# Kernel optimization log

Hardware: AMD Instinct MI355X
Metric: run time of the kernel (lower is better)

Reference implementation:

```python
import jax, jax.numpy as jnp
import numpy as np

NUM_USER = 50000
NUM_ITEM = 50000
DIM_FEAT = 4096
DIM_LATENT = 128
NUM_LAYER = 2
AVG_DEG = 16
N = NUM_USER + NUM_ITEM
E_HALF = NUM_USER * AVG_DEG  # user->item edges; reversed copies added too


def setup_inputs() -> dict:
    key = jax.random.key(0)
    ks = jax.random.split(key, 6)
    features = jax.random.normal(ks[0], (NUM_ITEM, DIM_FEAT), dtype=jnp.float32)
    # xavier_normal for preference: std = sqrt(2/(fan_in+fan_out))
    preference = jax.random.normal(ks[1], (NUM_USER, DIM_LATENT), dtype=jnp.float32) * np.sqrt(2.0 / (NUM_USER + DIM_LATENT)).astype(np.float32)
    W1 = jax.random.normal(ks[2], (DIM_FEAT, 4 * DIM_LATENT), dtype=jnp.float32) * np.float32(DIM_FEAT ** -0.5)
    b1 = jnp.zeros((4 * DIM_LATENT,), jnp.float32)
    W2 = jax.random.normal(ks[3], (4 * DIM_LATENT, DIM_LATENT), dtype=jnp.float32) * np.float32((4 * DIM_LATENT) ** -0.5)
    b2 = jnp.zeros((DIM_LATENT,), jnp.float32)
    # bipartite user-item edges, both directions; no self-loops by construction
    u = jax.random.randint(ks[4], (E_HALF,), 0, NUM_USER)
    it = jax.random.randint(ks[5], (E_HALF,), NUM_USER, N)
    src = jnp.concatenate([u, it])
    dst = jnp.concatenate([it, u])
    edge_index = jnp.stack([src, dst], axis=0)
    return {"features": features, "preference": preference, "W1": W1, "b1": b1,
            "W2": W2, "b2": b2, "edge_index": edge_index}


def reference(features, preference, W1, b1, W2, b2, edge_index):
    # proj MLP: Linear -> LeakyReLU(0.01) -> Linear
    item_feat = jax.nn.leaky_relu(features @ W1 + b1, negative_slope=0.01) @ W2 + b2
    x = jnp.concatenate([preference, item_feat], axis=0)  # [N, D]
    # F.normalize(x, dim=-1): divide by L2 norm clamped to 1e-12
    x = x / jnp.maximum(jnp.linalg.norm(x, axis=-1, keepdims=True), 1e-12)
    row, col = edge_index[0], edge_index[1]  # source (j), target (i)
    # degree over source index only, as in BaseGCN.message
    deg = jax.ops.segment_sum(jnp.ones(row.shape[0], dtype=x.dtype), row, num_segments=N)
    deg_inv_sqrt = deg ** -0.5  # endpoints all appear as sources, so finite on edges
    norm = deg_inv_sqrt[row] * deg_inv_sqrt[col]  # [E]
    out = x
    h = x
    for _ in range(NUM_LAYER):
        msg = norm[:, None] * h[row]                      # gather + scale [E, D]
        h = jax.ops.segment_sum(msg, col, num_segments=N)  # scatter-add [N, D]
        out = out + h
    return out, preference
```

## Files before the change

### kernel.cpp

```cpp
#include <hip/hip_runtime.h>

#define NUSER 50000
#define NITEM 50000
#define NTOT  100000
#define DFEAT 4096
#define DLAT  128
#define DHID  512
#define MTILES 391
#define MPAD  (MTILES*128)
#define G1TILES 782

typedef __attribute__((ext_vector_type(8))) short bf16x8;
typedef __attribute__((ext_vector_type(4))) float f32x4;

__device__ __forceinline__ ushort f2bf(float f) {
  union { float f; unsigned u; } in; in.f = f;
  unsigned u = in.u;
  u += 0x7fffu + ((u >> 16) & 1u);
  return (ushort)(u >> 16);
}
__device__ __forceinline__ unsigned pk2bf_fast(float lo, float hi) {
  unsigned ul = __float_as_uint(lo) + 0x8000u;
  unsigned uh = __float_as_uint(hi) + 0x8000u;
  return (ul >> 16) | (uh & 0xffff0000u);
}

__global__ __launch_bounds__(512) void gemm1_kernel(
    const float* __restrict__ A,
    const ushort* __restrict__ BT,
    const float* __restrict__ bias,
    ushort* __restrict__ Hid)
{
  extern __shared__ char smem[];
  char* AsC = smem;
  char* BsC = smem + 8192;

  const int tid = threadIdx.x;
  const int lane = tid & 63;
  const int wid = tid >> 6;
  const int row0 = blockIdx.x * 64;

  const int lr = lane & 15;
  const int kq = lane >> 4;
  const int l7 = lane & 7;

  f32x4 acc[4][4];
  const f32x4 z = {0.f, 0.f, 0.f, 0.f};
  #pragma unroll
  for (int m = 0; m < 4; ++m)
    #pragma unroll
    for (int n = 0; n < 4; ++n) acc[m][n] = z;

  const int r0 = tid >> 3, t0 = tid & 7;
  const int aswz = (t0 ^ (r0 & 7)) << 4;
  const size_t asrc = (size_t)(row0 + r0) * DFEAT + t0 * 8;
  char* adst = AsC + r0 * 128 + aswz;
  const bool aok = (row0 + r0) < NITEM;

  for (int k0 = 0; k0 < DFEAT; k0 += 64) {
    #pragma unroll
    for (int j = 0; j < 8; ++j) {
      int q = (wid * 8 + j) * 64 + lane;
      int r = q >> 3, t = q & 7;
      const ushort* src = BT + (size_t)r * DFEAT + k0 + ((t ^ (r & 7)) << 3);
      __builtin_amdgcn_global_load_lds(
          (const __attribute__((address_space(1))) void*)src,
          (__attribute__((address_space(3))) void*)(BsC + (size_t)(wid * 8 + j) * 1024),
          16, 0, 0);
    }
    {
      float4 v0 = make_float4(0.f, 0.f, 0.f, 0.f), v1 = v0;
      if (aok) {
        const float* s = A + asrc + k0;
        v0 = *(const float4*)s;
        v1 = *(const float4*)(s + 4);
      }
      uint4 p;
      p.x = pk2bf_fast(v0.x, v0.y); p.y = pk2bf_fast(v0.z, v0.w);
      p.z = pk2bf_fast(v1.x, v1.y); p.w = pk2bf_fast(v1.z, v1.w);
      *(uint4*)adst = p;
    }
    __syncthreads();

    #pragma unroll
    for (int kk = 0; kk < 2; ++kk) {
      const int c8 = kk * 4 + kq;
      const int sx = (c8 ^ l7) << 4;
      bf16x8 a[4], b[4];
      #pragma unroll
      for (int m = 0; m < 4; ++m)
        a[m] = *(const bf16x8*)(AsC + (m * 16 + lr) * 128 + sx);
      #pragma unroll
      for (int n = 0; n < 4; ++n)
        b[n] = *(const bf16x8*)(BsC + (wid * 64 + n * 16 + lr) * 128 + sx);
      #pragma unroll
      for (int m = 0; m < 4; ++m)
        #pragma unroll
        for (int n = 0; n < 4; ++n)
          acc[m][n] = __builtin_amdgcn_mfma_f32_16x16x32_bf16(a[m], b[n], acc[m][n], 0, 0, 0);
    }
    __syncthreads();
  }

  #pragma unroll
  for (int n = 0; n < 4; ++n) {
    int col = wid * 64 + n * 16 + lr;
    float bv = bias[col];
    #pragma unroll
    for (int m = 0; m < 4; ++m) {
      #pragma unroll
      for (int i = 0; i < 4; ++i) {
        int row = row0 + m * 16 + kq * 4 + i;
        float v = acc[m][n][i] + bv;
        v = v > 0.f ? v : 0.01f * v;
        Hid[(size_t)row * DHID + col] = f2bf(v);
      }
    }
  }
}

#define BM 128
#define BK 32
#define LDW 40

__global__ __launch_bounds__(256) void gemm2_kernel(
    const ushort* __restrict__ A,
    const ushort* __restrict__ BT,
    const float* __restrict__ bias,
    float* __restrict__ X)
{
  __shared__ ushort As[BM][LDW];
  __shared__ ushort Bs[BM][LDW];
  const int tid = threadIdx.x;
  const int lane = tid & 63;
  const int wid = tid >> 6;
  const int wr = wid >> 1, wc = wid & 1;
  const int row0 = blockIdx.x * BM;

  f32x4 acc[4][4];
  const f32x4 z = {0.f, 0.f, 0.f, 0.f};
  #pragma unroll
  for (int m = 0; m < 4; ++m)
    #pragma unroll
    for (int n = 0; n < 4; ++n) acc[m][n] = z;

  const int lrow = lane & 15;
  const int kb = (lane >> 4) * 8;

  for (int k0 = 0; k0 < DHID; k0 += BK) {
    #pragma unroll
    for (int j = 0; j < 2; ++j) {
      int idx = tid + j * 256;
      int r = idx >> 2;
      int c8 = (idx & 3) << 3;
      *(uint4*)&As[r][c8] = *(const uint4*)(A + (size_t)(row0 + r) * DHID + k0 + c8);
      *(uint4*)&Bs[r][c8] = *(const uint4*)(BT + (size_t)r * DHID + k0 + c8);
    }
    __syncthreads();
    bf16x8 a[4], b[4];
    #pragma unroll
    for (int m = 0; m < 4; ++m) a[m] = *(const bf16x8*)&As[wr * 64 + m * 16 + lrow][kb];
    #pragma unroll
    for (int n = 0; n < 4; ++n) b[n] = *(const bf16x8*)&Bs[wc * 64 + n * 16 + lrow][kb];
    #pragma unroll
    for (int m = 0; m < 4; ++m)
      #pragma unroll
      for (int n = 0; n < 4; ++n)
        acc[m][n] = __builtin_amdgcn_mfma_f32_16x16x32_bf16(a[m], b[n], acc[m][n], 0, 0, 0);
    __syncthreads();
  }
  #pragma unroll
  for (int n = 0; n < 4; ++n) {
    int col = wc * 64 + n * 16 + lrow;
    float bv = bias[col];
    #pragma unroll
    for (int m = 0; m < 4; ++m) {
      #pragma unroll
      for (int i = 0; i < 4; ++i) {
        int row = row0 + wr * 64 + m * 16 + (lane >> 4) * 4 + i;
        if (row < NITEM)
          X[(size_t)(NUSER + row) * DLAT + col] = acc[m][n][i] + bv;
      }
    }
  }
}

__global__ __launch_bounds__(256) void prep_w1t(const float* __restrict__ W1,
                                                ushort* __restrict__ W1T) {
  __shared__ ushort t[64][72];
  const int bx = blockIdx.x & 63;
  const int by = blockIdx.x >> 6;
  const int k0 = bx * 64, n0 = by * 64;
  const int tid = threadIdx.x;
  #pragma unroll
  for (int j = 0; j < 4; ++j) {
    int f = tid + j * 256;
    int r = f >> 4, c4 = (f & 15) << 2;
    float4 v = *(const float4*)(W1 + (size_t)(k0 + r) * DHID + n0 + c4);
    t[c4 + 0][r] = f2bf(v.x);
    t[c4 + 1][r] = f2bf(v.y);
    t[c4 + 2][r] = f2bf(v.z);
    t[c4 + 3][r] = f2bf(v.w);
  }
  __syncthreads();
  #pragma unroll
  for (int j = 0; j < 2; ++j) {
    int o = tid + j * 256;
    int r = o >> 3, c8 = (o & 7) << 3;
    *(uint4*)(W1T + (size_t)(n0 + r) * DFEAT + k0 + c8) = *(const uint4*)&t[r][c8];
  }
}
__global__ void prep_w2t(const float* __restrict__ W2, ushort* __restrict__ W2T) {
  int idx = blockIdx.x * 256 + threadIdx.x;
  int n = idx >> 9, k = idx & 511;
  W2T[idx] = f2bf(W2[(size_t)k * DLAT + n]);
}

__global__ __launch_bounds__(256) void normalize_kernel(
    const float* __restrict__ pref, float* __restrict__ X) {
  int gw = (blockIdx.x * 256 + threadIdx.x) >> 6;
  int lane = threadIdx.x & 63;
  if (gw >= NTOT) return;
  const float* src = (gw < NUSER) ? (pref + (size_t)gw * DLAT) : (X + (size_t)gw * DLAT);
  float2 v = *(const float2*)(src + lane * 2);
  float s = v.x * v.x + v.y * v.y;
  #pragma unroll
  for (int off = 32; off; off >>= 1) s += __shfl_xor(s, off, 64);
  float inv = 1.0f / fmaxf(sqrtf(s), 1e-12f);
  float2 o; o.x = v.x * inv; o.y = v.y * inv;
  *(float2*)(X + (size_t)gw * DLAT + lane * 2) = o;
}

__global__ void count_kernel(const int* __restrict__ col, int* __restrict__ cnt, int E) {
  int e = blockIdx.x * 256 + threadIdx.x;
  if (e < E) atomicAdd(&cnt[col[e]], 1);
}
__global__ void dinv_kernel(const int* __restrict__ cnt, float* __restrict__ dinv, int n) {
  int i = blockIdx.x * 256 + threadIdx.x;
  if (i < n) dinv[i] = rsqrtf((float)cnt[i]);
}

#define SCAN_NB ((NTOT + 1023) / 1024)
__global__ __launch_bounds__(1024) void scan1_kernel(const int* __restrict__ cnt,
                                                     int* __restrict__ off,
                                                     int* __restrict__ bsum, int n) {
  __shared__ int ws[16];
  __shared__ int wexcl[16];
  const int tid = threadIdx.x, lane = tid & 63, wv = tid >> 6;
  int i = blockIdx.x * 1024 + tid;
  int v = (i < n) ? cnt[i] : 0;
  int x = v;
  #pragma unroll
  for (int o = 1; o < 64; o <<= 1) {
    int t = __shfl_up(x, o, 64);
    if (lane >= o) x += t;
  }
  if (lane == 63) ws[wv] = x;
  __syncthreads();
  if (tid < 16) {
    int y = ws[tid];
    #pragma unroll
    for (int o = 1; o < 16; o <<= 1) {
      int t = __shfl_up(y, o, 64);
      if (tid >= o) y += t;
    }
    wexcl[tid] = y - ws[tid];
    if (tid == 15) bsum[blockIdx.x] = y;
  }
  __syncthreads();
  if (i < n) off[i] = wexcl[wv] + (x - v);
}
__global__ __launch_bounds__(128) void scan2_kernel(int* __restrict__ bsum,
                                                    int* __restrict__ off, int nb, int n) {
  __shared__ int ws[2];
  const int tid = threadIdx.x, lane = tid & 63, wv = tid >> 6;
  int v = (tid < nb) ? bsum[tid] : 0;
  int x = v;
  #pragma unroll
  for (int o = 1; o < 64; o <<= 1) {
    int t = __shfl_up(x, o, 64);
    if (lane >= o) x += t;
  }
  if (lane == 63) ws[wv] = x;
  __syncthreads();
  int excl_w = (wv == 1) ? ws[0] : 0;
  if (tid < nb) bsum[tid] = excl_w + (x - v);
  if (tid == nb - 1) off[n] = excl_w + x;
}
__global__ __launch_bounds__(1024) void scan3_kernel(int* __restrict__ off,
                                                     const int* __restrict__ bsum, int n) {
  int i = blockIdx.x * 1024 + threadIdx.x;
  if (i < n) off[i] += bsum[blockIdx.x];
}

__global__ void fill_kernel(const int* __restrict__ row, const int* __restrict__ col,
                            const float* __restrict__ dinv, const int* __restrict__ off,
                            int* __restrict__ cur, int2* __restrict__ srcw, int E) {
  int e = blockIdx.x * 256 + threadIdx.x;
  if (e >= E) return;
  int r = row[e], c = col[e];
  float w = dinv[r] * dinv[c];
  int p = atomicAdd(&cur[c], 1);
  int2 pk; pk.x = r; pk.y = __float_as_int(w);
  srcw[off[c] + p] = pk;
}

template <int FINAL>
__global__ __launch_bounds__(256) void spmm_kernel(
    const int2* __restrict__ srcw, const int* __restrict__ off,
    const float* __restrict__ h, float* __restrict__ hout,
    const float* __restrict__ addA, const float* __restrict__ addB) {
  int node = (int)((blockIdx.x * 256 + threadIdx.x) >> 6);
  int lane = threadIdx.x & 63;
  if (node >= NTOT) return;
  int p = off[node], pend = off[node + 1];
  float ax = 0.f, ay = 0.f;
  for (; p + 3 < pend; p += 4) {
    int2 e0 = srcw[p];
    int2 e1 = srcw[p + 1];
    int2 e2 = srcw[p + 2];
    int2 e3 = srcw[p + 3];
    float2 v0 = *(const float2*)(h + (size_t)e0.x * DLAT + lane * 2);
    float2 v1 = *(const float2*)(h + (size_t)e1.x * DLAT + lane * 2);
    float2 v2 = *(const float2*)(h + (size_t)e2.x * DLAT + lane * 2);
    float2 v3 = *(const float2*)(h + (size_t)e3.x * DLAT + lane * 2);
    float w0 = __int_as_float(e0.y), w1 = __int_as_float(e1.y);
    float w2 = __int_as_float(e2.y), w3 = __int_as_float(e3.y);
    ax += w0 * v0.x + w1 * v1.x + w2 * v2.x + w3 * v3.x;
    ay += w0 * v0.y + w1 * v1.y + w2 * v2.y + w3 * v3.y;
  }
  for (; p < pend; ++p) {
    int2 e0 = srcw[p];
    float w0 = __int_as_float(e0.y);
    float2 v0 = *(const float2*)(h + (size_t)e0.x * DLAT + lane * 2);
    ax += w0 * v0.x;
    ay += w0 * v0.y;
  }
  size_t o = (size_t)node * DLAT + lane * 2;
  if (FINAL) {
    float2 a = *(const float2*)(addA + o);
    float2 b = *(const float2*)(addB + o);
    ax += a.x + b.x;
    ay += a.y + b.y;
  }
  float2 r; r.x = ax; r.y = ay;
  *(float2*)(hout + o) = r;
}

extern "C" void kernel_launch(void* const* d_in, const int* in_sizes, int n_in,
                              void* d_out, int out_size, void* d_ws, size_t ws_size,
                              hipStream_t stream) {
  const float* features  = (const float*)d_in[0];
  const float* preference = (const float*)d_in[1];
  const float* W1 = (const float*)d_in[2];
  const float* b1 = (const float*)d_in[3];
  const float* W2 = (const float*)d_in[4];
  const float* b2 = (const float*)d_in[5];
  const int*   edges = (const int*)d_in[6];
  const int E = in_sizes[6] / 2;
  const int* erow = edges;
  const int* ecol = edges + E;
  float* out = (float*)d_out;

  char* ws = (char*)d_ws;
  size_t off_b = 0;
  auto alloc = [&](size_t bytes) {
    void* p = ws + off_b;
    off_b = (off_b + bytes + 255) & ~(size_t)255;
    return p;
  };
  ushort* W1T  = (ushort*)alloc((size_t)DHID * DFEAT * 2);
  ushort* W2T  = (ushort*)alloc((size_t)DLAT * DHID * 2);
  ushort* Hid  = (ushort*)alloc((size_t)MPAD * DHID * 2);
  float*  X    = (float*)alloc((size_t)NTOT * DLAT * 4);
  float*  hA   = (float*)alloc((size_t)NTOT * DLAT * 4);
  int*    cnt  = (int*)alloc((size_t)NTOT * 4);
  int*    offs = (int*)alloc((size_t)(NTOT + 1) * 4);
  int*    cur  = (int*)alloc((size_t)NTOT * 4);
  float*  dinv = (float*)alloc((size_t)NTOT * 4);
  int*    bsum = (int*)alloc((size_t)SCAN_NB * 4);
  int2*   srcw = (int2*)alloc((size_t)E * 8);

  prep_w1t<<<512, 256, 0, stream>>>(W1, W1T);
  prep_w2t<<<(DLAT * DHID) / 256, 256, 0, stream>>>(W2, W2T);
  gemm1_kernel<<<G1TILES, 512, 72 * 1024, stream>>>(features, W1T, b1, Hid);
  gemm2_kernel<<<MTILES, 256, 0, stream>>>(Hid, W2T, b2, X);
  normalize_kernel<<<(NTOT * 64 + 255) / 256, 256, 0, stream>>>(preference, X);

  hipMemsetAsync(cnt, 0, (size_t)NTOT * 4, stream);
  count_kernel<<<(E + 255) / 256, 256, 0, stream>>>(ecol, cnt, E);
  dinv_kernel<<<(NTOT + 255) / 256, 256, 0, stream>>>(cnt, dinv, NTOT);
  scan1_kernel<<<SCAN_NB, 1024, 0, stream>>>(cnt, offs, bsum, NTOT);
  scan2_kernel<<<1, 128, 0, stream>>>(bsum, offs, SCAN_NB, NTOT);
  scan3_kernel<<<SCAN_NB, 1024, 0, stream>>>(offs, bsum, NTOT);
  hipMemsetAsync(cur, 0, (size_t)NTOT * 4, stream);
  fill_kernel<<<(E + 255) / 256, 256, 0, stream>>>(erow, ecol, dinv, offs, cur, srcw, E);

  spmm_kernel<0><<<(NTOT * 64 + 255) / 256, 256, 0, stream>>>(srcw, offs, X, hA, nullptr, nullptr);
  spmm_kernel<1><<<(NTOT * 64 + 255) / 256, 256, 0, stream>>>(srcw, offs, hA, out, X, hA);

  hipMemcpyAsync(out + (size_t)NTOT * DLAT, preference, (size_t)NUSER * DLAT * 4,
                 hipMemcpyDeviceToDevice, stream);
}
```

Before: 823.7 us.

## Double-buffer GEMM1 LDS tiles and gather bf16 embeddings in SpMM

```diff
diff --git a/kernel.cpp b/kernel.cpp
--- a/kernel.cpp
+++ b/kernel.cpp
@@ -24,6 +24,8 @@
   unsigned uh = __float_as_uint(hi) + 0x8000u;
   return (ul >> 16) | (uh & 0xffff0000u);
 }
+__device__ __forceinline__ float bflo(unsigned u) { return __uint_as_float(u << 16); }
+__device__ __forceinline__ float bfhi(unsigned u) { return __uint_as_float(u & 0xffff0000u); }
 
 __global__ __launch_bounds__(512) void gemm1_kernel(
     const float* __restrict__ A,
@@ -32,8 +34,10 @@
     ushort* __restrict__ Hid)
 {
   extern __shared__ char smem[];
-  char* AsC = smem;
-  char* BsC = smem + 8192;
+  char* AsC0 = smem;
+  char* AsC1 = smem + 8192;
+  char* BsC0 = smem + 16384;
+  char* BsC1 = smem + 16384 + 65536;
 
   const int tid = threadIdx.x;
   const int lane = tid & 63;
@@ -52,12 +56,11 @@
     for (int n = 0; n < 4; ++n) acc[m][n] = z;
 
   const int r0 = tid >> 3, t0 = tid & 7;
-  const int aswz = (t0 ^ (r0 & 7)) << 4;
+  const int aoff = r0 * 128 + ((t0 ^ (r0 & 7)) << 4);
   const size_t asrc = (size_t)(row0 + r0) * DFEAT + t0 * 8;
-  char* adst = AsC + r0 * 128 + aswz;
   const bool aok = (row0 + r0) < NITEM;
 
-  for (int k0 = 0; k0 < DFEAT; k0 += 64) {
+  auto stageB = [&](char* dstB, int k0) {
     #pragma unroll
     for (int j = 0; j < 8; ++j) {
       int q = (wid * 8 + j) * 64 + lane;
@@ -65,23 +68,11 @@
       const ushort* src = BT + (size_t)r * DFEAT + k0 + ((t ^ (r & 7)) << 3);
       __builtin_amdgcn_global_load_lds(
           (const __attribute__((address_space(1))) void*)src,
-          (__attribute__((address_space(3))) void*)(BsC + (size_t)(wid * 8 + j) * 1024),
+          (__attribute__((address_space(3))) void*)(dstB + (size_t)(wid * 8 + j) * 1024),
           16, 0, 0);
     }
-    {
-      float4 v0 = make_float4(0.f, 0.f, 0.f, 0.f), v1 = v0;
-      if (aok) {
-        const float* s = A + asrc + k0;
-        v0 = *(const float4*)s;
-        v1 = *(const float4*)(s + 4);
-      }
-      uint4 p;
-      p.x = pk2bf_fast(v0.x, v0.y); p.y = pk2bf_fast(v0.z, v0.w);
-      p.z = pk2bf_fast(v1.x, v1.y); p.w = pk2bf_fast(v1.z, v1.w);
-      *(uint4*)adst = p;
-    }
-    __syncthreads();
-
+  };
+  auto compute = [&](const char* AsC, const char* BsC) {
     #pragma unroll
     for (int kk = 0; kk < 2; ++kk) {
       const int c8 = kk * 4 + kq;
@@ -99,8 +90,47 @@
         for (int n = 0; n < 4; ++n)
           acc[m][n] = __builtin_amdgcn_mfma_f32_16x16x32_bf16(a[m], b[n], acc[m][n], 0, 0, 0);
     }
+  };
+
+  stageB(BsC0, 0);
+  {
+    float4 v0 = make_float4(0.f, 0.f, 0.f, 0.f), v1 = v0;
+    if (aok) {
+      const float* s = A + asrc;
+      v0 = *(const float4*)s; v1 = *(const float4*)(s + 4);
+    }
+    uint4 p;
+    p.x = pk2bf_fast(v0.x, v0.y); p.y = pk2bf_fast(v0.z, v0.w);
+    p.z = pk2bf_fast(v1.x, v1.y); p.w = pk2bf_fast(v1.z, v1.w);
+    *(uint4*)(AsC0 + aoff) = p;
+  }
+  __syncthreads();
+
+  for (int t = 0; t < 63; ++t) {
+    const int cur = t & 1;
+    char* As = cur ? AsC1 : AsC0;
+    char* Bs = cur ? BsC1 : BsC0;
+    char* Asn = cur ? AsC0 : AsC1;
+    char* Bsn = cur ? BsC0 : BsC1;
+    const int k1 = (t + 1) * 64;
+
+    stageB(Bsn, k1);
+    float4 v0 = make_float4(0.f, 0.f, 0.f, 0.f), v1 = v0;
+    if (aok) {
+      const float* s = A + asrc + k1;
+      v0 = *(const float4*)s; v1 = *(const float4*)(s + 4);
+    }
+
+    compute(As, Bs);
+
+    uint4 p;
+    p.x = pk2bf_fast(v0.x, v0.y); p.y = pk2bf_fast(v0.z, v0.w);
+    p.z = pk2bf_fast(v1.x, v1.y); p.w = pk2bf_fast(v1.z, v1.w);
+    *(uint4*)(Asn + aoff) = p;
+
     __syncthreads();
   }
+  compute(AsC1, BsC1);
 
   #pragma unroll
   for (int n = 0; n < 4; ++n) {
@@ -217,7 +247,8 @@
 }
 
 __global__ __launch_bounds__(256) void normalize_kernel(
-    const float* __restrict__ pref, float* __restrict__ X) {
+    const float* __restrict__ pref, float* __restrict__ X,
+    unsigned* __restrict__ Xb) {
   int gw = (blockIdx.x * 256 + threadIdx.x) >> 6;
   int lane = threadIdx.x & 63;
   if (gw >= NTOT) return;
@@ -229,6 +260,7 @@
   float inv = 1.0f / fmaxf(sqrtf(s), 1e-12f);
   float2 o; o.x = v.x * inv; o.y = v.y * inv;
   *(float2*)(X + (size_t)gw * DLAT + lane * 2) = o;
+  Xb[(size_t)gw * 64 + lane] = pk2bf_fast(o.x, o.y);
 }
 
 __global__ void count_kernel(const int* __restrict__ col, int* __restrict__ cnt, int E) {
@@ -308,7 +340,8 @@
 template <int FINAL>
 __global__ __launch_bounds__(256) void spmm_kernel(
     const int2* __restrict__ srcw, const int* __restrict__ off,
-    const float* __restrict__ h, float* __restrict__ hout,
+    const unsigned* __restrict__ hb, float* __restrict__ hout,
+    unsigned* __restrict__ houtb,
     const float* __restrict__ addA, const float* __restrict__ addB) {
   int node = (int)((blockIdx.x * 256 + threadIdx.x) >> 6);
   int lane = threadIdx.x & 63;
@@ -320,21 +353,21 @@
     int2 e1 = srcw[p + 1];
     int2 e2 = srcw[p + 2];
     int2 e3 = srcw[p + 3];
-    float2 v0 = *(const float2*)(h + (size_t)e0.x * DLAT + lane * 2);
-    float2 v1 = *(const float2*)(h + (size_t)e1.x * DLAT + lane * 2);
-    float2 v2 = *(const float2*)(h + (size_t)e2.x * DLAT + lane * 2);
-    float2 v3 = *(const float2*)(h + (size_t)e3.x * DLAT + lane * 2);
+    unsigned u0 = hb[(size_t)e0.x * 64 + lane];
+    unsigned u1 = hb[(size_t)e1.x * 64 + lane];
+    unsigned u2 = hb[(size_t)e2.x * 64 + lane];
+    unsigned u3 = hb[(size_t)e3.x * 64 + lane];
     float w0 = __int_as_float(e0.y), w1 = __int_as_float(e1.y);
     float w2 = __int_as_float(e2.y), w3 = __int_as_float(e3.y);
-    ax += w0 * v0.x + w1 * v1.x + w2 * v2.x + w3 * v3.x;
-    ay += w0 * v0.y + w1 * v1.y + w2 * v2.y + w3 * v3.y;
+    ax += w0 * bflo(u0) + w1 * bflo(u1) + w2 * bflo(u2) + w3 * bflo(u3);
+    ay += w0 * bfhi(u0) + w1 * bfhi(u1) + w2 * bfhi(u2) + w3 * bfhi(u3);
   }
   for (; p < pend; ++p) {
     int2 e0 = srcw[p];
     float w0 = __int_as_float(e0.y);
-    float2 v0 = *(const float2*)(h + (size_t)e0.x * DLAT + lane * 2);
-    ax += w0 * v0.x;
-    ay += w0 * v0.y;
+    unsigned u0 = hb[(size_t)e0.x * 64 + lane];
+    ax += w0 * bflo(u0);
+    ay += w0 * bfhi(u0);
   }
   size_t o = (size_t)node * DLAT + lane * 2;
   if (FINAL) {
@@ -342,6 +375,8 @@
     float2 b = *(const float2*)(addB + o);
     ax += a.x + b.x;
     ay += a.y + b.y;
+  } else {
+    houtb[(size_t)node * 64 + lane] = pk2bf_fast(ax, ay);
   }
   float2 r; r.x = ax; r.y = ay;
   *(float2*)(hout + o) = r;
@@ -369,23 +404,25 @@
     off_b = (off_b + bytes + 255) & ~(size_t)255;
     return p;
   };
-  ushort* W1T  = (ushort*)alloc((size_t)DHID * DFEAT * 2);
-  ushort* W2T  = (ushort*)alloc((size_t)DLAT * DHID * 2);
-  ushort* Hid  = (ushort*)alloc((size_t)MPAD * DHID * 2);
-  float*  X    = (float*)alloc((size_t)NTOT * DLAT * 4);
-  float*  hA   = (float*)alloc((size_t)NTOT * DLAT * 4);
-  int*    cnt  = (int*)alloc((size_t)NTOT * 4);
-  int*    offs = (int*)alloc((size_t)(NTOT + 1) * 4);
-  int*    cur  = (int*)alloc((size_t)NTOT * 4);
-  float*  dinv = (float*)alloc((size_t)NTOT * 4);
-  int*    bsum = (int*)alloc((size_t)SCAN_NB * 4);
-  int2*   srcw = (int2*)alloc((size_t)E * 8);
+  ushort*   W1T  = (ushort*)alloc((size_t)DHID * DFEAT * 2);
+  ushort*   W2T  = (ushort*)alloc((size_t)DLAT * DHID * 2);
+  ushort*   Hid  = (ushort*)alloc((size_t)MPAD * DHID * 2);
+  float*    X    = (float*)alloc((size_t)NTOT * DLAT * 4);
+  float*    hA   = (float*)alloc((size_t)NTOT * DLAT * 4);
+  unsigned* Xb   = (unsigned*)alloc((size_t)NTOT * 64 * 4);
+  unsigned* hAb  = (unsigned*)alloc((size_t)NTOT * 64 * 4);
+  int*      cnt  = (int*)alloc((size_t)NTOT * 4);
+  int*      offs = (int*)alloc((size_t)(NTOT + 1) * 4);
+  int*      cur  = (int*)alloc((size_t)NTOT * 4);
+  float*    dinv = (float*)alloc((size_t)NTOT * 4);
+  int*      bsum = (int*)alloc((size_t)SCAN_NB * 4);
+  int2*     srcw = (int2*)alloc((size_t)E * 8);
 
   prep_w1t<<<512, 256, 0, stream>>>(W1, W1T);
   prep_w2t<<<(DLAT * DHID) / 256, 256, 0, stream>>>(W2, W2T);
-  gemm1_kernel<<<G1TILES, 512, 72 * 1024, stream>>>(features, W1T, b1, Hid);
+  gemm1_kernel<<<G1TILES, 512, 144 * 1024, stream>>>(features, W1T, b1, Hid);
   gemm2_kernel<<<MTILES, 256, 0, stream>>>(Hid, W2T, b2, X);
-  normalize_kernel<<<(NTOT * 64 + 255) / 256, 256, 0, stream>>>(preference, X);
+  normalize_kernel<<<(NTOT * 64 + 255) / 256, 256, 0, stream>>>(preference, X, Xb);
 
   hipMemsetAsync(cnt, 0, (size_t)NTOT * 4, stream);
   count_kernel<<<(E + 255) / 256, 256, 0, stream>>>(ecol, cnt, E);
@@ -396,8 +433,8 @@
   hipMemsetAsync(cur, 0, (size_t)NTOT * 4, stream);
   fill_kernel<<<(E + 255) / 256, 256, 0, stream>>>(erow, ecol, dinv, offs, cur, srcw, E);
 
-  spmm_kernel<0><<<(NTOT * 64 + 255) / 256, 256, 0, stream>>>(srcw, offs, X, hA, nullptr, nullptr);
-  spmm_kernel<1><<<(NTOT * 64 + 255) / 256, 256, 0, stream>>>(srcw, offs, hA, out, X, hA);
+  spmm_kernel<0><<<(NTOT * 64 + 255) / 256, 256, 0, stream>>>(srcw, offs, Xb, hA, hAb, nullptr, nullptr);
+  spmm_kernel<1><<<(NTOT * 64 + 255) / 256, 256, 0, stream>>>(srcw, offs, hAb, out, nullptr, X, hA);
 
   hipMemcpyAsync(out + (size_t)NTOT * DLAT, preference, (size_t)NUSER * DLAT * 4,
                  hipMemcpyDeviceToDevice, stream);
```

Result: slower. 895.7 us (+8.7%).
